# Kernel tuning notes

Measured on AMD Instinct MI355X. Metric: run time of the kernel, lower is better.

## Reference

```python
import jax, jax.numpy as jnp
from jax import lax
import numpy as np

LSTM = 128      # encoder hidden per direction
H2 = 2 * LSTM   # decoder hidden / bi-encoder output dim
E = 1024        # embedding dim
V = 30611       # vocab
A = 64          # attention dim
B, S, T = 16, 400, 96
START_TOK = 101


def setup_inputs() -> dict:
    key = jax.random.key(0)
    ks = jax.random.split(key, 24)
    d = {}
    d["word_embedding"] = jax.random.normal(ks[0], (V, E), jnp.float32) * 0.05
    d["article"] = jax.random.randint(ks[1], (B, S), 0, V)
    d["article_length"] = jax.random.randint(ks[2], (B,), S // 2, S + 1)
    d["abstract"] = jax.random.randint(ks[3], (B, T), 0, V)

    def p(k, shape, scale):
        return jax.random.normal(k, shape, jnp.float32) * scale

    # encoder BiLSTM (PyTorch gate order i,f,g,o), forward and backward dirs
    d["enc_Wih_f"] = p(ks[4], (4 * LSTM, E), 0.03)
    d["enc_Whh_f"] = p(ks[5], (4 * LSTM, LSTM), 0.08)
    d["enc_b_f"] = jnp.zeros((4 * LSTM,), jnp.float32)
    d["enc_Wih_b"] = p(ks[6], (4 * LSTM, E), 0.03)
    d["enc_Whh_b"] = p(ks[7], (4 * LSTM, LSTM), 0.08)
    d["enc_b_b"] = jnp.zeros((4 * LSTM,), jnp.float32)
    # decoder LSTM: input = embed(1024) + context(256)
    d["dec_Wih"] = p(ks[8], (4 * H2, E + H2), 0.03)
    d["dec_Whh"] = p(ks[9], (4 * H2, H2), 0.06)
    d["dec_b"] = jnp.zeros((4 * H2,), jnp.float32)
    # vocab prediction
    d["pred_W"] = p(ks[10], (V, H2), 0.06)
    d["pred_b"] = jnp.zeros((V,), jnp.float32)
    # additive attention
    d["attn_s_W"] = p(ks[11], (A, H2), 0.06)
    d["attn_s_b"] = jnp.zeros((A,), jnp.float32)
    d["attn_h_W"] = p(ks[12], (A, H2), 0.06)
    d["attn_h_b"] = jnp.zeros((A,), jnp.float32)
    d["attn_f_W"] = p(ks[13], (1, A), 0.12)
    d["attn_f_b"] = jnp.zeros((1,), jnp.float32)
    return d


def _lstm_cell(x, h, c, Wih, Whh, b):
    g = x @ Wih.T + h @ Whh.T + b
    i, f, gg, o = jnp.split(g, 4, axis=-1)
    c = jax.nn.sigmoid(f) * c + jax.nn.sigmoid(i) * jnp.tanh(gg)
    h = jax.nn.sigmoid(o) * jnp.tanh(c)
    return h, c


def reference(word_embedding, article, article_length, abstract,
              enc_Wih_f, enc_Whh_f, enc_b_f, enc_Wih_b, enc_Whh_b, enc_b_b,
              dec_Wih, dec_Whh, dec_b, pred_W, pred_b,
              attn_s_W, attn_s_b, attn_h_W, attn_h_b, attn_f_W, attn_f_b):
    dt = word_embedding.dtype
    # ---- encoder ----
    xe = word_embedding[article]          # [B,S,E]
    xs = xe.transpose(1, 0, 2)            # [S,B,E]
    z = jnp.zeros((B, LSTM), dt)

    def fstep(carry, x):
        h, c = carry
        h, c = _lstm_cell(x, h, c, enc_Wih_f, enc_Whh_f, enc_b_f)
        return (h, c), h

    def bstep(carry, x):
        h, c = carry
        h, c = _lstm_cell(x, h, c, enc_Wih_b, enc_Whh_b, enc_b_b)
        return (h, c), h

    (hf, cf_f), out_f = lax.scan(fstep, (z, z), xs)
    (hb, cf_b), out_b = lax.scan(bstep, (z, z), xs, reverse=True)
    enc_out = jnp.concatenate([out_f, out_b], axis=-1).transpose(1, 0, 2)  # [B,S,2H]

    # decoder init state = concat of final fwd/bwd encoder states
    h0 = jnp.concatenate([hf, hb], axis=-1)   # [B,H2]
    c0 = jnp.concatenate([cf_f, cf_b], axis=-1)

    # attention mask: (+9999 valid, -9999 pad); min(score, mask) keeps valid scores
    length = jnp.clip(article_length, 1, S)
    pos = jnp.arange(S)
    mask = jnp.where(pos[None, :] < length[:, None], 9999.0, -9999.0).astype(dt)

    enc_ws = enc_out @ attn_s_W.T + attn_s_b  # [B,S,A], precomputed per original code

    # teacher forcing inputs: step 0 uses token 101, step t uses abstract[:, t-1]
    tokens_in = jnp.concatenate(
        [jnp.full((B, 1), START_TOK, dtype=abstract.dtype), abstract[:, :-1]], axis=1)
    emb_in = word_embedding[tokens_in].transpose(1, 0, 2)  # [T,B,E]

    def dstep(carry, emb):
        h, c, ctx = carry
        x = jnp.concatenate([emb, ctx], axis=-1)           # [B,E+H2]
        h, c = _lstm_cell(x, h, c, dec_Wih, dec_Whh, dec_b)
        logits = h @ pred_W.T + pred_b                     # [B,V]
        wh = h @ attn_h_W.T + attn_h_b                     # [B,A]
        score = jnp.tanh(enc_ws + wh[:, None, :]) @ attn_f_W[0] + attn_f_b[0]  # [B,S]
        score = jnp.minimum(score, mask)
        w = jax.nn.softmax(score, axis=-1)
        ctx = jnp.einsum('bs,bsd->bd', w, enc_out)         # [B,H2]
        return (h, c, ctx), logits

    ctx0 = jnp.zeros((B, H2), dt)
    _, logits = lax.scan(dstep, (h0, c0, ctx0), emb_in)    # [T,B,V]

    logits = logits.transpose(1, 0, 2).reshape(B * T, V)
    tgt = abstract.reshape(-1)
    logp = jax.nn.log_softmax(logits, axis=-1)
    nll = -jnp.take_along_axis(logp, tgt[:, None], axis=1)[:, 0]
    valid = (tgt != 0).astype(logits.dtype)                # ignore_index=0
    loss = jnp.sum(nll * valid) / jnp.maximum(jnp.sum(valid), 1.0)
    return loss
```

## Files before the change

### kernel.cpp

```cpp
#include <hip/hip_runtime.h>
#include <cmath>

#define NB 16
#define SS 400
#define TT 96
#define HL 128
#define HH 256
#define AA 64
#define VV 30611
#define VVP 30720
#define START_TOK 101
#define NCHUNK 120

typedef __attribute__((ext_vector_type(8))) short bf16x8;
typedef __attribute__((ext_vector_type(4))) float f32x4;

#define PIN4(v) asm volatile("" : "+v"((v).x), "+v"((v).y), "+v"((v).z), "+v"((v).w))
#define LBAR() asm volatile("s_waitcnt lgkmcnt(0)\n\ts_barrier" ::: "memory")

__device__ __forceinline__ float gload(const float* p) {
  return __hip_atomic_load(p, __ATOMIC_RELAXED, __HIP_MEMORY_SCOPE_AGENT);
}
__device__ __forceinline__ void gstore(float* p, float v) {
  __hip_atomic_store(p, v, __ATOMIC_RELAXED, __HIP_MEMORY_SCOPE_AGENT);
}
__device__ __forceinline__ float sigmf(float x) { return 1.0f / (1.0f + __expf(-x)); }
__device__ __forceinline__ float tanhf_(float x) {
  float xc = fminf(fmaxf(x, -15.0f), 15.0f);
  return 1.0f - 2.0f / (__expf(2.0f * xc) + 1.0f);
}
__device__ __forceinline__ short f2bf(float f) {
  unsigned u = __float_as_uint(f);
  unsigned r = (u + 0x7FFFu + ((u >> 16) & 1u)) >> 16;
  return (short)r;
}
__device__ __forceinline__ void flagbar(int* flags, int b, int g, int target) {
  __syncthreads();
  if (threadIdx.x == 0)
    __hip_atomic_store(&flags[b*8 + g], target, __ATOMIC_RELAXED, __HIP_MEMORY_SCOPE_AGENT);
  if (threadIdx.x < 8) {
    while (__hip_atomic_load(&flags[b*8 + threadIdx.x], __ATOMIC_RELAXED, __HIP_MEMORY_SCOPE_AGENT) < target)
      __builtin_amdgcn_s_sleep(1);
  }
  LBAR();
}

__global__ __launch_bounds__(256) void k_init(int* flags) {
  if (threadIdx.x < 128) flags[threadIdx.x] = 0;
}

__global__ __launch_bounds__(256) void k_casts(
    const float* __restrict__ predW, const float* __restrict__ wf,
    const float* __restrict__ wb, const float* __restrict__ dwih,
    short* __restrict__ predWb, short* __restrict__ wfB,
    short* __restrict__ wbB, short* __restrict__ dwB)
{
  const int stride = gridDim.x * 256;
  const int t0 = blockIdx.x * 256 + threadIdx.x;
  for (int i = t0; i < VVP*256; i += stride)
    predWb[i] = (i < VV*256) ? f2bf(predW[i]) : (short)0;
  for (int i = t0; i < 512*1024; i += stride) wfB[i] = f2bf(wf[i]);
  for (int i = t0; i < 512*1024; i += stride) wbB[i] = f2bf(wb[i]);
  for (int i = t0; i < 1024*1024; i += stride) {
    int r = i >> 10, k = i & 1023;
    dwB[i] = f2bf(dwih[r*1280 + k]);
  }
}

__global__ __launch_bounds__(256) void k_embproj_enc_mfma(
    const float* __restrict__ emb, const int* __restrict__ article,
    const short* __restrict__ wfB, const short* __restrict__ wbB,
    const float* __restrict__ bf, const float* __restrict__ bb,
    float* __restrict__ xcomb)
{
  const int m0 = blockIdx.x * 64;
  const int n0 = blockIdx.y * 256;
  const int t = threadIdx.x;
  const int w = t >> 6, l = t & 63;
  __shared__ short Abuf[64*136];
  __shared__ int tok[64];
  if (t < 64) {
    int R = m0 + t, s = R >> 4, b = R & 15;
    tok[t] = article[b*SS + s];
  }
  const short* __restrict__ Wb = (n0 < 512) ? wfB : wbB;
  const int nb0 = (n0 < 512) ? n0 : (n0 - 512);
  f32x4 acc[4][4];
  #pragma unroll
  for (int i = 0; i < 4; ++i)
    #pragma unroll
    for (int j = 0; j < 4; ++j) acc[i][j] = (f32x4){0.f,0.f,0.f,0.f};
  __syncthreads();
  const int ar = t >> 2, ak0 = (t & 3) * 32;
  for (int kc = 0; kc < 8; ++kc) {
    const float* src = emb + (size_t)tok[ar]*1024 + kc*128 + ak0;
    #pragma unroll
    for (int j = 0; j < 8; ++j) {
      float4 v = *(const float4*)(src + 4*j);
      short4 s4; s4.x = f2bf(v.x); s4.y = f2bf(v.y); s4.z = f2bf(v.z); s4.w = f2bf(v.w);
      *(short4*)(&Abuf[ar*136 + ak0 + 4*j]) = s4;
    }
    LBAR();
    #pragma unroll
    for (int ks = 0; ks < 4; ++ks) {
      bf16x8 af[4];
      #pragma unroll
      for (int mr = 0; mr < 4; ++mr)
        af[mr] = *(const bf16x8*)(&Abuf[(mr*16 + (l & 15))*136 + ks*32 + (l >> 4)*8]);
      #pragma unroll
      for (int ct = 0; ct < 4; ++ct) {
        int n = nb0 + w*64 + ct*16 + (l & 15);
        bf16x8 bfr = *(const bf16x8*)(Wb + (size_t)n*1024 + kc*128 + ks*32 + (l >> 4)*8);
        #pragma unroll
        for (int mr = 0; mr < 4; ++mr)
          acc[mr][ct] = __builtin_amdgcn_mfma_f32_16x16x32_bf16(af[mr], bfr, acc[mr][ct], 0, 0, 0);
      }
    }
    LBAR();
  }
  #pragma unroll
  for (int ct = 0; ct < 4; ++ct) {
    int n = n0 + w*64 + ct*16 + (l & 15);
    float bias = (n < 512) ? bf[n] : bb[n - 512];
    #pragma unroll
    for (int mr = 0; mr < 4; ++mr) {
      #pragma unroll
      for (int r = 0; r < 4; ++r) {
        int R = m0 + mr*16 + (l >> 4)*4 + r;
        xcomb[(size_t)R*1024 + n] = acc[mr][ct][r] + bias;
      }
    }
  }
}

__global__ __launch_bounds__(256) void k_embproj_dec_mfma(
    const float* __restrict__ emb, const int* __restrict__ abstr,
    const short* __restrict__ dwB, const float* __restrict__ db,
    float* __restrict__ decpre)
{
  const int m0 = blockIdx.x * 64;
  const int n0 = blockIdx.y * 256;
  const int t = threadIdx.x;
  const int w = t >> 6, l = t & 63;
  __shared__ short Abuf[64*136];
  __shared__ int tok[64];
  if (t < 64) {
    int R = m0 + t, tt = R >> 4, b = R & 15;
    tok[t] = (tt == 0) ? START_TOK : abstr[b*TT + tt - 1];
  }
  f32x4 acc[4][4];
  #pragma unroll
  for (int i = 0; i < 4; ++i)
    #pragma unroll
    for (int j = 0; j < 4; ++j) acc[i][j] = (f32x4){0.f,0.f,0.f,0.f};
  __syncthreads();
  const int ar = t >> 2, ak0 = (t & 3) * 32;
  for (int kc = 0; kc < 8; ++kc) {
    const float* src = emb + (size_t)tok[ar]*1024 + kc*128 + ak0;
    #pragma unroll
    for (int j = 0; j < 8; ++j) {
      float4 v = *(const float4*)(src + 4*j);
      short4 s4; s4.x = f2bf(v.x); s4.y = f2bf(v.y); s4.z = f2bf(v.z); s4.w = f2bf(v.w);
      *(short4*)(&Abuf[ar*136 + ak0 + 4*j]) = s4;
    }
    LBAR();
    #pragma unroll
    for (int ks = 0; ks < 4; ++ks) {
      bf16x8 af[4];
      #pragma unroll
      for (int mr = 0; mr < 4; ++mr)
        af[mr] = *(const bf16x8*)(&Abuf[(mr*16 + (l & 15))*136 + ks*32 + (l >> 4)*8]);
      #pragma unroll
      for (int ct = 0; ct < 4; ++ct) {
        int n = n0 + w*64 + ct*16 + (l & 15);
        bf16x8 bfr = *(const bf16x8*)(dwB + (size_t)n*1024 + kc*128 + ks*32 + (l >> 4)*8);
        #pragma unroll
        for (int mr = 0; mr < 4; ++mr)
          acc[mr][ct] = __builtin_amdgcn_mfma_f32_16x16x32_bf16(af[mr], bfr, acc[mr][ct], 0, 0, 0);
      }
    }
    LBAR();
  }
  #pragma unroll
  for (int ct = 0; ct < 4; ++ct) {
    int n = n0 + w*64 + ct*16 + (l & 15);
    float bias = db[n];
    #pragma unroll
    for (int mr = 0; mr < 4; ++mr) {
      #pragma unroll
      for (int r = 0; r < 4; ++r) {
        int R = m0 + mr*16 + (l >> 4)*4 + r;
        decpre[(size_t)R*1024 + n] = acc[mr][ct][r] + bias;
      }
    }
  }
}

__global__ __launch_bounds__(1024, 4) void k_encoder(
    const float* __restrict__ xcomb,
    const float* __restrict__ whhf, const float* __restrict__ whhb,
    float* __restrict__ encout,
    float* __restrict__ hpub,
    float* __restrict__ c0buf)
{
  const int b = blockIdx.x & 15, dir = blockIdx.x >> 4;
  const int t = threadIdx.x;
  const int row = t & 511;
  const int ks = t >> 9;
  const float* __restrict__ Whh = dir ? whhb : whhf;
  float4 wr[16];
  #pragma unroll
  for (int j = 0; j < 16; ++j) {
    wr[j] = *(const float4*)(Whh + row*128 + ks*64 + j*4);
    PIN4(wr[j]);
  }
  __shared__ float hl[128];
  __shared__ float part[2][512];
  float c_reg = 0.0f;
  if (t < 128) hl[t] = 0.0f;
  float xv0 = 0.f, xv1 = 0.f, xv2 = 0.f, xv3 = 0.f;
  if (t < 128) {
    const float* xr = xcomb + ((dir ? (SS-1) : 0)*NB + b)*1024 + dir*512 + t;
    xv0 = xr[0]; xv1 = xr[128]; xv2 = xr[256]; xv3 = xr[384];
  }
  __syncthreads();
  for (int s = 0; s < SS; ++s) {
    const int sf = dir ? (SS-1-s) : s;
    const float* hs = hl + ks*64;
    float a0 = 0.f, a1 = 0.f, a2 = 0.f, a3 = 0.f;
    #pragma unroll
    for (int j = 0; j < 16; j += 4) {
      float4 h0 = *(const float4*)(hs + j*4);
      float4 h1 = *(const float4*)(hs + j*4 + 4);
      float4 h2 = *(const float4*)(hs + j*4 + 8);
      float4 h3 = *(const float4*)(hs + j*4 + 12);
      a0 += wr[j].x*h0.x + wr[j].y*h0.y + wr[j].z*h0.z + wr[j].w*h0.w;
      a1 += wr[j+1].x*h1.x + wr[j+1].y*h1.y + wr[j+1].z*h1.z + wr[j+1].w*h1.w;
      a2 += wr[j+2].x*h2.x + wr[j+2].y*h2.y + wr[j+2].z*h2.z + wr[j+2].w*h2.w;
      a3 += wr[j+3].x*h3.x + wr[j+3].y*h3.y + wr[j+3].z*h3.z + wr[j+3].w*h3.w;
    }
    part[ks][row] = (a0 + a1) + (a2 + a3);
    float nx0 = 0.f, nx1 = 0.f, nx2 = 0.f, nx3 = 0.f;
    if (t < 128 && s + 1 < SS) {
      const int sfn = dir ? (SS-2-s) : (s+1);
      const float* xr = xcomb + (sfn*NB + b)*1024 + dir*512 + t;
      nx0 = xr[0]; nx1 = xr[128]; nx2 = xr[256]; nx3 = xr[384];
    }
    LBAR();
    if (t < 128) {
      float gi = part[0][t]       + part[1][t]       + xv0;
      float gf = part[0][128 + t] + part[1][128 + t] + xv1;
      float gg = part[0][256 + t] + part[1][256 + t] + xv2;
      float go = part[0][384 + t] + part[1][384 + t] + xv3;
      float iv = sigmf(gi), fv = sigmf(gf), gv = tanhf_(gg), ov = sigmf(go);
      c_reg = fv*c_reg + iv*gv;
      float hv = ov*tanhf_(c_reg);
      hl[t] = hv;
      encout[(b*SS + sf)*HH + dir*HL + t] = hv;
    }
    LBAR();
    xv0 = nx0; xv1 = nx1; xv2 = nx2; xv3 = nx3;
  }
  if (t < 128) {
    hpub[b*HH + dir*HL + t] = hl[t];
    c0buf[b*HH + dir*HL + t] = c_reg;
  }
}

__global__ __launch_bounds__(256) void k_encws(
    const float* __restrict__ encout,
    const float* __restrict__ asW, const float* __restrict__ asb,
    float* __restrict__ encwsR)
{
  const int rt = blockIdx.x;
  const int tid = threadIdx.x;
  __shared__ float Al[32*260];
  #pragma unroll
  for (int i = 0; i < 32; ++i) {
    int l = tid + i*256;
    int r = l >> 8, k = l & 255;
    Al[r*260 + k] = encout[(rt*32 + r)*256 + k];
  }
  __syncthreads();
  const int a = tid & 63, rg = tid >> 6;
  float acc[8];
  #pragma unroll
  for (int q = 0; q < 8; ++q) acc[q] = 0.0f;
  const float4* w4 = (const float4*)(asW + a*256);
  for (int k4 = 0; k4 < 64; ++k4) {
    float4 w = w4[k4];
    #pragma unroll
    for (int q = 0; q < 8; ++q) {
      const float4* a4 = (const float4*)(Al + (rg*8 + q)*260);
      float4 av = a4[k4];
      acc[q] += av.x*w.x + av.y*w.y + av.z*w.z + av.w*w.w;
    }
  }
  float bias = asb[a];
  #pragma unroll
  for (int q = 0; q < 8; ++q) {
    int row = rt*32 + rg*8 + q;
    encwsR[row*64 + a] = acc[q] + bias;
  }
}

__global__ __launch_bounds__(1024, 4) void k_decoder(
    const float* __restrict__ decpre,
    const float* __restrict__ dwhh,
    const float* __restrict__ dwih,
    const float* __restrict__ ahW, const float* __restrict__ ahb,
    const float* __restrict__ afW, const float* __restrict__ afb,
    const float* __restrict__ encwsR,
    const float* __restrict__ encout,
    const int* __restrict__ alen,
    const float* __restrict__ c0buf,
    float* hpub,
    float* cpub,
    float* wpub,
    float* __restrict__ dhall,
    int* flags)
{
  const int wg = blockIdx.x;
  const int g = wg >> 4, b = wg & 15;
  const int t = threadIdx.x;
  const int r = t & 127, ks = t >> 7;
  const int lane = t & 63;
  const int u = t & 31;
  const int s0 = g*50;

  const int grow = (r >> 5)*256 + g*32 + (r & 31);
  float4 wr[16];
  #pragma unroll
  for (int j = 0; j < 16; ++j) {
    int k = ks*64 + j*4;
    wr[j] = (k < 256) ? *(const float4*)(dwhh + grow*256 + k)
                      : *(const float4*)(dwih + grow*1280 + 1024 + (k - 256));
    PIN4(wr[j]);
  }

  __shared__ float encl[50*256];
  __shared__ float wsl[50*68];
  __shared__ float ahWt[256*68];
  __shared__ float hc[512];
  __shared__ float part[8][132];
  __shared__ float wh[64];
  __shared__ float fwl[64];
  __shared__ float scl[64];
  __shared__ float sh_m, sh_s;

  for (int i = t; i < 50*256; i += 1024) {
    int si = i >> 8, d = i & 255;
    encl[i] = encout[(b*SS + s0 + si)*HH + d];
  }
  for (int i = t; i < 50*64; i += 1024) {
    int si = i >> 6, a = i & 63;
    wsl[si*68 + a] = encwsR[(b*SS + s0 + si)*64 + a];
  }
  for (int i = t; i < 64*256; i += 1024) {
    int a = i >> 8, k = i & 255;
    ahWt[k*68 + a] = ahW[i];
  }
  if (t < 64) fwl[t] = afW[t];
  const float fb0 = afb[0];
  int len = alen[b]; len = min(max(len, 1), SS);
  float c_reg = 0.f;
  float pre0 = 0.f, pre1 = 0.f, pre2 = 0.f, pre3 = 0.f;
  if (t < 256) {
    c_reg = c0buf[b*HH + g*32 + u];
    hc[t] = gload(hpub + b*HH + t);
    hc[256 + t] = 0.0f;
    const float* pr = decpre + (size_t)(0*NB + b)*1024 + g*32 + u;
    pre0 = pr[0]; pre1 = pr[256]; pre2 = pr[512]; pre3 = pr[768];
  }
  __syncthreads();

  for (int tt = 0; tt < TT; ++tt) {
    {
      const float* hs = hc + ks*64;
      float a0 = 0.f, a1 = 0.f, a2 = 0.f, a3 = 0.f;
      #pragma unroll
      for (int j = 0; j < 16; j += 4) {
        float4 h0 = *(const float4*)(hs + j*4);
        float4 h1 = *(const float4*)(hs + j*4 + 4);
        float4 h2 = *(const float4*)(hs + j*4 + 8);
        float4 h3 = *(const float4*)(hs + j*4 + 12);
        a0 += wr[j].x*h0.x + wr[j].y*h0.y + wr[j].z*h0.z + wr[j].w*h0.w;
        a1 += wr[j+1].x*h1.x + wr[j+1].y*h1.y + wr[j+1].z*h1.z + wr[j+1].w*h1.w;
        a2 += wr[j+2].x*h2.x + wr[j+2].y*h2.y + wr[j+2].z*h2.z + wr[j+2].w*h2.w;
        a3 += wr[j+3].x*h3.x + wr[j+3].y*h3.y + wr[j+3].z*h3.z + wr[j+3].w*h3.w;
      }
      part[ks][r] = (a0 + a1) + (a2 + a3);
    }
    LBAR();
    if (t < 256) {
      float g0 = pre0, g1 = pre1, g2 = pre2, g3 = pre3;
      #pragma unroll
      for (int j = 0; j < 8; ++j) {
        g0 += part[j][u];
        g1 += part[j][32 + u];
        g2 += part[j][64 + u];
        g3 += part[j][96 + u];
      }
      float iv = sigmf(g0), fv = sigmf(g1), gv = tanhf_(g2), ov = sigmf(g3);
      c_reg = fv*c_reg + iv*gv;
      float hv = ov*tanhf_(c_reg);
      if (t < 32) {
        gstore(hpub + b*HH + g*32 + t, hv);
        dhall[(tt*NB + b)*HH + g*32 + t] = hv;
      }
      int wv = t >> 6;
      int a = wv*16 + (lane >> 2);
      int j4 = lane & 3;
      float wacc = 0.f;
      #pragma unroll
      for (int i = 0; i < 8; ++i) {
        int u2 = j4*8 + i;
        float hx = __shfl(hv, u2, 64);
        wacc += ahWt[(g*32 + u2)*68 + a] * hx;
      }
      wacc += __shfl_xor(wacc, 1);
      wacc += __shfl_xor(wacc, 2);
      if (j4 == 0) gstore(wpub + (b*8 + g)*72 + a, wacc);
    }
    flagbar(flags, b, g, 2*tt + 1);
    if (t < 256) {
      hc[t] = gload(hpub + b*HH + t);
      if (tt + 1 < TT) {
        const float* pr = decpre + (size_t)((tt+1)*NB + b)*1024 + g*32 + u;
        pre0 = pr[0]; pre1 = pr[256]; pre2 = pr[512]; pre3 = pr[768];
      }
    } else if (t < 320) {
      int a = t - 256;
      float s = ahb[a];
      #pragma unroll
      for (int j = 0; j < 8; ++j) s += gload(wpub + (b*8 + j)*72 + a);
      wh[a] = s;
    }
    LBAR();
    if (t < 800) {
      int s = t >> 4, j = t & 15;
      const float* wrow = wsl + s*68 + j*4;
      float p = fwl[j*4]   * tanhf_(wrow[0] + wh[j*4])
              + fwl[j*4+1] * tanhf_(wrow[1] + wh[j*4+1])
              + fwl[j*4+2] * tanhf_(wrow[2] + wh[j*4+2])
              + fwl[j*4+3] * tanhf_(wrow[3] + wh[j*4+3]);
      p += __shfl_xor(p, 1);
      p += __shfl_xor(p, 2);
      p += __shfl_xor(p, 4);
      p += __shfl_xor(p, 8);
      if (j == 0) scl[s] = p;
    }
    LBAR();
    if (t < 64) {
      float sc = -1e30f;
      if (t < 50) {
        sc = fb0 + scl[t];
        sc = fminf(sc, (s0 + t < len) ? 9999.0f : -9999.0f);
      }
      float m = sc;
      #pragma unroll
      for (int o = 32; o; o >>= 1) m = fmaxf(m, __shfl_xor(m, o));
      float p = (t < 50) ? __expf(sc - m) : 0.0f;
      scl[t] = p;
      float ssum = p;
      #pragma unroll
      for (int o = 32; o; o >>= 1) ssum += __shfl_xor(ssum, o);
      if (t == 0) { sh_m = m; sh_s = ssum; }
    }
    LBAR();
    if (t < 256) {
      float acc = 0.0f;
      const float* eb = encl + t;
      #pragma unroll 10
      for (int i = 0; i < 50; ++i) acc += scl[i] * eb[i*256];
      gstore(cpub + (b*8 + g)*272 + t, acc);
      if (t == 0) gstore(cpub + (b*8 + g)*272 + 256, sh_m);
      if (t == 1) gstore(cpub + (b*8 + g)*272 + 257, sh_s);
    }
    flagbar(flags, b, g, 2*tt + 2);
    if (t < 256) {
      float mj[8], sj[8];
      #pragma unroll
      for (int j = 0; j < 8; ++j) {
        mj[j] = gload(cpub + (b*8 + j)*272 + 256);
        sj[j] = gload(cpub + (b*8 + j)*272 + 257);
      }
      float M = mj[0];
      #pragma unroll
      for (int j = 1; j < 8; ++j) M = fmaxf(M, mj[j]);
      float denom = 0.f, ctx = 0.f;
      #pragma unroll
      for (int j = 0; j < 8; ++j) {
        float e = __expf(mj[j] - M);
        denom += sj[j] * e;
        ctx += gload(cpub + (b*8 + j)*272 + t) * e;
      }
      hc[256 + t] = ctx / denom;
    }
    LBAR();
  }
}

__global__ __launch_bounds__(256) void k_pred_mfma(
    const float* __restrict__ dhall,
    const short* __restrict__ predWb,
    const float* __restrict__ predb,
    float* __restrict__ pm, float* __restrict__ ps)
{
  const int m0 = blockIdx.x * 64;
  const int ch = blockIdx.y;
  const int c0 = ch * 256;
  const int t = threadIdx.x;
  const int w = t >> 6, l = t & 63;
  __shared__ __align__(16) char smem[64*264*4];
  short* Abuf = (short*)smem;
  float* L    = (float*)smem;
  __shared__ float red[256];
  __shared__ float rowmax[64];

  {
    const int ar = t >> 2, ak0 = (t & 3) * 64;
    const float* src = dhall + (size_t)(m0 + ar)*256 + ak0;
    #pragma unroll
    for (int j = 0; j < 16; ++j) {
      float4 v = *(const float4*)(src + 4*j);
      short4 s4; s4.x = f2bf(v.x); s4.y = f2bf(v.y); s4.z = f2bf(v.z); s4.w = f2bf(v.w);
      *(short4*)(&Abuf[ar*264 + ak0 + 4*j]) = s4;
    }
  }
  LBAR();
  f32x4 acc[4][4];
  #pragma unroll
  for (int i = 0; i < 4; ++i)
    #pragma unroll
    for (int j = 0; j < 4; ++j) acc[i][j] = (f32x4){0.f,0.f,0.f,0.f};
  #pragma unroll
  for (int kst = 0; kst < 8; ++kst) {
    bf16x8 af[4];
    #pragma unroll
    for (int mr = 0; mr < 4; ++mr)
      af[mr] = *(const bf16x8*)(&Abuf[(mr*16 + (l & 15))*264 + kst*32 + (l >> 4)*8]);
    #pragma unroll
    for (int ct = 0; ct < 4; ++ct) {
      int col = c0 + w*64 + ct*16 + (l & 15);
      bf16x8 bfr = *(const bf16x8*)(predWb + (size_t)col*256 + kst*32 + (l >> 4)*8);
      #pragma unroll
      for (int mr = 0; mr < 4; ++mr)
        acc[mr][ct] = __builtin_amdgcn_mfma_f32_16x16x32_bf16(af[mr], bfr, acc[mr][ct], 0, 0, 0);
    }
  }
  LBAR();
  #pragma unroll
  for (int ct = 0; ct < 4; ++ct) {
    int col = c0 + w*64 + ct*16 + (l & 15);
    float bias = (col < VV) ? predb[col] : 0.0f;
    bool valid = (col < VV);
    #pragma unroll
    for (int mr = 0; mr < 4; ++mr) {
      #pragma unroll
      for (int r = 0; r < 4; ++r) {
        int rl = mr*16 + (l >> 4)*4 + r;
        L[rl*264 + w*64 + ct*16 + (l & 15)] = valid ? (acc[mr][ct][r] + bias) : -1e30f;
      }
    }
  }
  LBAR();
  {
    const int row = t & 63, qd = t >> 6;
    float m = -1e30f;
    const float* Lr = L + row*264 + qd*64;
    for (int i = 0; i < 64; ++i) m = fmaxf(m, Lr[i]);
    red[qd*64 + row] = m;
  }
  LBAR();
  if (t < 64) {
    float m = fmaxf(fmaxf(red[t], red[64+t]), fmaxf(red[128+t], red[192+t]));
    rowmax[t] = m;
  }
  LBAR();
  {
    const int row = t & 63, qd = t >> 6;
    float m = rowmax[row];
    float ssum = 0.f;
    const float* Lr = L + row*264 + qd*64;
    for (int i = 0; i < 64; ++i) ssum += __expf(Lr[i] - m);
    red[qd*64 + row] = ssum;
  }
  LBAR();
  if (t < 64) {
    float ssum = red[t] + red[64+t] + red[128+t] + red[192+t];
    pm[(m0 + t)*NCHUNK + ch] = rowmax[t];
    ps[(m0 + t)*NCHUNK + ch] = ssum;
  }
}

__global__ __launch_bounds__(256) void k_loss_part(
    const float* __restrict__ pm, const float* __restrict__ ps,
    const float* __restrict__ dhall,
    const float* __restrict__ predW, const float* __restrict__ predb,
    const int* __restrict__ abstr, float* __restrict__ lpart)
{
  const int tid = threadIdx.x;
  const int row = blockIdx.x*256 + tid;
  __shared__ float rs[256], rc[256];
  float lsum = 0.0f, lcnt = 0.0f;
  {
    int t = row >> 4, b = row & 15;
    int tok = abstr[b*TT + t];
    float m = -1e30f;
    for (int c = 0; c < NCHUNK; ++c) m = fmaxf(m, pm[row*NCHUNK + c]);
    float ss = 0.0f;
    for (int c = 0; c < NCHUNK; ++c) ss += ps[row*NCHUNK + c] * __expf(pm[row*NCHUNK + c] - m);
    float lse = m + __logf(ss);
    float tl = predb[tok];
    const float* hrow = dhall + row*256;
    const float* wrow = predW + tok*256;
    #pragma unroll 4
    for (int k = 0; k < 256; ++k) tl += hrow[k] * wrow[k];
    if (tok != 0) { lsum = lse - tl; lcnt = 1.0f; }
  }
  rs[tid] = lsum; rc[tid] = lcnt;
  __syncthreads();
  for (int st = 128; st; st >>= 1) {
    if (tid < st) { rs[tid] += rs[tid + st]; rc[tid] += rc[tid + st]; }
    __syncthreads();
  }
  if (tid == 0) { lpart[blockIdx.x*2] = rs[0]; lpart[blockIdx.x*2 + 1] = rc[0]; }
}

__global__ void k_loss_final(const float* __restrict__ lpart, float* __restrict__ out) {
  if (threadIdx.x == 0) {
    float s = 0.f, c = 0.f;
    for (int i = 0; i < 6; ++i) { s += lpart[i*2]; c += lpart[i*2 + 1]; }
    out[0] = s / fmaxf(c, 1.0f);
  }
}

extern "C" void kernel_launch(void* const* d_in, const int* in_sizes, int n_in,
                              void* d_out, int out_size, void* d_ws, size_t ws_size,
                              hipStream_t stream) {
  const float* emb   = (const float*)d_in[0];
  const int* article = (const int*)d_in[1];
  const int* alen    = (const int*)d_in[2];
  const int* abstr   = (const int*)d_in[3];
  const float* eWihF = (const float*)d_in[4];
  const float* eWhhF = (const float*)d_in[5];
  const float* ebF   = (const float*)d_in[6];
  const float* eWihB = (const float*)d_in[7];
  const float* eWhhB = (const float*)d_in[8];
  const float* ebB   = (const float*)d_in[9];
  const float* dWih  = (const float*)d_in[10];
  const float* dWhh  = (const float*)d_in[11];
  const float* db    = (const float*)d_in[12];
  const float* pW    = (const float*)d_in[13];
  const float* pb    = (const float*)d_in[14];
  const float* asW   = (const float*)d_in[15];
  const float* asb   = (const float*)d_in[16];
  const float* ahW   = (const float*)d_in[17];
  const float* ahb   = (const float*)d_in[18];
  const float* afW   = (const float*)d_in[19];
  const float* afb   = (const float*)d_in[20];
  float* out = (float*)d_out;

  float* w = (float*)d_ws;
  size_t o = 0;
  float* xcomb  = w + o; o += (size_t)SS*NB*1024;
  float* encout = w + o; o += (size_t)NB*SS*HH;
  float* encwsR = w + o; o += (size_t)NB*SS*AA;
  float* decpre = w + o; o += (size_t)TT*NB*1024;
  float* dhall  = w + o; o += (size_t)TT*NB*HH;
  float* hpub   = w + o; o += NB*HH;
  float* cpub   = w + o; o += NB*8*272;
  float* wpub   = w + o; o += NB*8*72;
  float* c0buf  = w + o; o += NB*HH;
  float* pm     = w + o; o += (size_t)TT*NB*NCHUNK;
  float* ps     = w + o; o += (size_t)TT*NB*NCHUNK;
  float* lpart  = w + o; o += 16;
  int* flags = (int*)(w + o); o += 128;
  short* predWb = (short*)(w + o); o += (size_t)VVP*256/2;
  short* wfB    = (short*)(w + o); o += 512*1024/2;
  short* wbB    = (short*)(w + o); o += 512*1024/2;
  short* dwB    = (short*)(w + o); o += 1024*1024/2;

  k_init<<<1, 256, 0, stream>>>(flags);
  k_casts<<<2048, 256, 0, stream>>>(pW, eWihF, eWihB, dWih, predWb, wfB, wbB, dwB);
  k_embproj_enc_mfma<<<dim3(100, 4), 256, 0, stream>>>(emb, article, wfB, wbB, ebF, ebB, xcomb);
  k_embproj_dec_mfma<<<dim3(24, 4), 256, 0, stream>>>(emb, abstr, dwB, db, decpre);
  k_encoder<<<32, 1024, 0, stream>>>(xcomb, eWhhF, eWhhB, encout, hpub, c0buf);
  k_encws<<<200, 256, 0, stream>>>(encout, asW, asb, encwsR);
  k_decoder<<<128, 1024, 0, stream>>>(decpre, dWhh, dWih, ahW, ahb, afW, afb,
                                      encwsR, encout, alen, c0buf, hpub, cpub, wpub, dhall, flags);
  k_pred_mfma<<<dim3(24, 120), 256, 0, stream>>>(dhall, predWb, pb, pm, ps);
  k_loss_part<<<6, 256, 0, stream>>>(pm, ps, dhall, pW, pb, abstr, lpart);
  k_loss_final<<<1, 64, 0, stream>>>(lpart, out);
}
```

Measured before the change: 1.715 ms.

## Overlap vocab projection with decoder via flag-synced persistent blocks; shuffle-based encoder cell

```diff
diff --git a/kernel.cpp b/kernel.cpp
--- a/kernel.cpp
+++ b/kernel.cpp
@@ -19,6 +19,9 @@
 #define LBAR() asm volatile("s_waitcnt lgkmcnt(0)\n\ts_barrier" ::: "memory")
 
 __device__ __forceinline__ float gload(const float* p) {
+  return __hip_atomic_load(p, __ATOMIC_RELAXED, __HIP_MEMORY_SCOPE_AGENT);
+}
+__device__ __forceinline__ int gload_i(const int* p) {
   return __hip_atomic_load(p, __ATOMIC_RELAXED, __HIP_MEMORY_SCOPE_AGENT);
 }
 __device__ __forceinline__ void gstore(float* p, float v) {
@@ -205,28 +208,28 @@
 {
   const int b = blockIdx.x & 15, dir = blockIdx.x >> 4;
   const int t = threadIdx.x;
-  const int row = t & 511;
-  const int ks = t >> 9;
+  const int w = t >> 6, lane = t & 63;
+  const int kh = lane >> 5;
+  const int gate = (lane >> 3) & 3;
+  const int ul = lane & 7;
+  const int u = w*8 + ul;
+  const int row = gate*128 + u;
   const float* __restrict__ Whh = dir ? whhb : whhf;
   float4 wr[16];
   #pragma unroll
   for (int j = 0; j < 16; ++j) {
-    wr[j] = *(const float4*)(Whh + row*128 + ks*64 + j*4);
+    wr[j] = *(const float4*)(Whh + row*128 + kh*64 + j*4);
     PIN4(wr[j]);
   }
-  __shared__ float hl[128];
-  __shared__ float part[2][512];
-  float c_reg = 0.0f;
-  if (t < 128) hl[t] = 0.0f;
-  float xv0 = 0.f, xv1 = 0.f, xv2 = 0.f, xv3 = 0.f;
-  if (t < 128) {
-    const float* xr = xcomb + ((dir ? (SS-1) : 0)*NB + b)*1024 + dir*512 + t;
-    xv0 = xr[0]; xv1 = xr[128]; xv2 = xr[256]; xv3 = xr[384];
-  }
+  __shared__ float hl[2][128];
+  if (t < 128) hl[0][t] = 0.0f;
+  float c_reg = 0.0f, hlast = 0.0f;
+  float xv = xcomb[((dir ? (SS-1) : 0)*NB + b)*1024 + dir*512 + row];
   __syncthreads();
+  int p = 0;
   for (int s = 0; s < SS; ++s) {
     const int sf = dir ? (SS-1-s) : s;
-    const float* hs = hl + ks*64;
+    const float* hs = hl[p] + kh*64;
     float a0 = 0.f, a1 = 0.f, a2 = 0.f, a3 = 0.f;
     #pragma unroll
     for (int j = 0; j < 16; j += 4) {
@@ -239,31 +242,31 @@
       a2 += wr[j+2].x*h2.x + wr[j+2].y*h2.y + wr[j+2].z*h2.z + wr[j+2].w*h2.w;
       a3 += wr[j+3].x*h3.x + wr[j+3].y*h3.y + wr[j+3].z*h3.z + wr[j+3].w*h3.w;
     }
-    part[ks][row] = (a0 + a1) + (a2 + a3);
-    float nx0 = 0.f, nx1 = 0.f, nx2 = 0.f, nx3 = 0.f;
-    if (t < 128 && s + 1 < SS) {
+    float acc = (a0 + a1) + (a2 + a3);
+    float nxv = 0.f;
+    if (s + 1 < SS) {
       const int sfn = dir ? (SS-2-s) : (s+1);
-      const float* xr = xcomb + (sfn*NB + b)*1024 + dir*512 + t;
-      nx0 = xr[0]; nx1 = xr[128]; nx2 = xr[256]; nx3 = xr[384];
-    }
-    LBAR();
-    if (t < 128) {
-      float gi = part[0][t]       + part[1][t]       + xv0;
-      float gf = part[0][128 + t] + part[1][128 + t] + xv1;
-      float gg = part[0][256 + t] + part[1][256 + t] + xv2;
-      float go = part[0][384 + t] + part[1][384 + t] + xv3;
-      float iv = sigmf(gi), fv = sigmf(gf), gv = tanhf_(gg), ov = sigmf(go);
+      nxv = xcomb[(sfn*NB + b)*1024 + dir*512 + row];
+    }
+    float full = acc + __shfl_xor(acc, 32) + xv;
+    float gf = __shfl(full, 8 + ul);
+    float gg = __shfl(full, 16 + ul);
+    float go = __shfl(full, 24 + ul);
+    if (lane < 8) {
+      float iv = sigmf(full), fv = sigmf(gf), gv = tanhf_(gg), ov = sigmf(go);
       c_reg = fv*c_reg + iv*gv;
       float hv = ov*tanhf_(c_reg);
-      hl[t] = hv;
-      encout[(b*SS + sf)*HH + dir*HL + t] = hv;
+      hl[p^1][u] = hv;
+      hlast = hv;
+      encout[(b*SS + sf)*HH + dir*HL + u] = hv;
     }
     LBAR();
-    xv0 = nx0; xv1 = nx1; xv2 = nx2; xv3 = nx3;
-  }
-  if (t < 128) {
-    hpub[b*HH + dir*HL + t] = hl[t];
-    c0buf[b*HH + dir*HL + t] = c_reg;
+    p ^= 1;
+    xv = nxv;
+  }
+  if (lane < 8) {
+    hpub[b*HH + dir*HL + u] = hlast;
+    c0buf[b*HH + dir*HL + u] = c_reg;
   }
 }
 
@@ -304,7 +307,7 @@
   }
 }
 
-__global__ __launch_bounds__(1024, 4) void k_decoder(
+__global__ __launch_bounds__(1024, 4) void k_decoder_pred(
     const float* __restrict__ decpre,
     const float* __restrict__ dwhh,
     const float* __restrict__ dwih,
@@ -314,283 +317,282 @@
     const float* __restrict__ encout,
     const int* __restrict__ alen,
     const float* __restrict__ c0buf,
-    float* hpub,
-    float* cpub,
-    float* wpub,
+    float* hpub, float* cpub, float* wpub,
     float* __restrict__ dhall,
-    int* flags)
-{
-  const int wg = blockIdx.x;
-  const int g = wg >> 4, b = wg & 15;
-  const int t = threadIdx.x;
-  const int r = t & 127, ks = t >> 7;
-  const int lane = t & 63;
-  const int u = t & 31;
-  const int s0 = g*50;
-
-  const int grow = (r >> 5)*256 + g*32 + (r & 31);
-  float4 wr[16];
-  #pragma unroll
-  for (int j = 0; j < 16; ++j) {
-    int k = ks*64 + j*4;
-    wr[j] = (k < 256) ? *(const float4*)(dwhh + grow*256 + k)
-                      : *(const float4*)(dwih + grow*1280 + 1024 + (k - 256));
-    PIN4(wr[j]);
-  }
-
-  __shared__ float encl[50*256];
-  __shared__ float wsl[50*68];
-  __shared__ float ahWt[256*68];
-  __shared__ float hc[512];
-  __shared__ float part[8][132];
-  __shared__ float wh[64];
-  __shared__ float fwl[64];
-  __shared__ float scl[64];
-  __shared__ float sh_m, sh_s;
-
-  for (int i = t; i < 50*256; i += 1024) {
-    int si = i >> 8, d = i & 255;
-    encl[i] = encout[(b*SS + s0 + si)*HH + d];
-  }
-  for (int i = t; i < 50*64; i += 1024) {
-    int si = i >> 6, a = i & 63;
-    wsl[si*68 + a] = encwsR[(b*SS + s0 + si)*64 + a];
-  }
-  for (int i = t; i < 64*256; i += 1024) {
-    int a = i >> 8, k = i & 255;
-    ahWt[k*68 + a] = ahW[i];
-  }
-  if (t < 64) fwl[t] = afW[t];
-  const float fb0 = afb[0];
-  int len = alen[b]; len = min(max(len, 1), SS);
-  float c_reg = 0.f;
-  float pre0 = 0.f, pre1 = 0.f, pre2 = 0.f, pre3 = 0.f;
-  if (t < 256) {
-    c_reg = c0buf[b*HH + g*32 + u];
-    hc[t] = gload(hpub + b*HH + t);
-    hc[256 + t] = 0.0f;
-    const float* pr = decpre + (size_t)(0*NB + b)*1024 + g*32 + u;
-    pre0 = pr[0]; pre1 = pr[256]; pre2 = pr[512]; pre3 = pr[768];
-  }
-  __syncthreads();
-
-  for (int tt = 0; tt < TT; ++tt) {
-    {
-      const float* hs = hc + ks*64;
-      float a0 = 0.f, a1 = 0.f, a2 = 0.f, a3 = 0.f;
-      #pragma unroll
-      for (int j = 0; j < 16; j += 4) {
-        float4 h0 = *(const float4*)(hs + j*4);
-        float4 h1 = *(const float4*)(hs + j*4 + 4);
-        float4 h2 = *(const float4*)(hs + j*4 + 8);
-        float4 h3 = *(const float4*)(hs + j*4 + 12);
-        a0 += wr[j].x*h0.x + wr[j].y*h0.y + wr[j].z*h0.z + wr[j].w*h0.w;
-        a1 += wr[j+1].x*h1.x + wr[j+1].y*h1.y + wr[j+1].z*h1.z + wr[j+1].w*h1.w;
-        a2 += wr[j+2].x*h2.x + wr[j+2].y*h2.y + wr[j+2].z*h2.z + wr[j+2].w*h2.w;
-        a3 += wr[j+3].x*h3.x + wr[j+3].y*h3.y + wr[j+3].z*h3.z + wr[j+3].w*h3.w;
-      }
-      part[ks][r] = (a0 + a1) + (a2 + a3);
-    }
-    LBAR();
-    if (t < 256) {
-      float g0 = pre0, g1 = pre1, g2 = pre2, g3 = pre3;
-      #pragma unroll
-      for (int j = 0; j < 8; ++j) {
-        g0 += part[j][u];
-        g1 += part[j][32 + u];
-        g2 += part[j][64 + u];
-        g3 += part[j][96 + u];
-      }
-      float iv = sigmf(g0), fv = sigmf(g1), gv = tanhf_(g2), ov = sigmf(g3);
-      c_reg = fv*c_reg + iv*gv;
-      float hv = ov*tanhf_(c_reg);
-      if (t < 32) {
-        gstore(hpub + b*HH + g*32 + t, hv);
-        dhall[(tt*NB + b)*HH + g*32 + t] = hv;
-      }
-      int wv = t >> 6;
-      int a = wv*16 + (lane >> 2);
-      int j4 = lane & 3;
-      float wacc = 0.f;
-      #pragma unroll
-      for (int i = 0; i < 8; ++i) {
-        int u2 = j4*8 + i;
-        float hx = __shfl(hv, u2, 64);
-        wacc += ahWt[(g*32 + u2)*68 + a] * hx;
-      }
-      wacc += __shfl_xor(wacc, 1);
-      wacc += __shfl_xor(wacc, 2);
-      if (j4 == 0) gstore(wpub + (b*8 + g)*72 + a, wacc);
-    }
-    flagbar(flags, b, g, 2*tt + 1);
-    if (t < 256) {
-      hc[t] = gload(hpub + b*HH + t);
-      if (tt + 1 < TT) {
-        const float* pr = decpre + (size_t)((tt+1)*NB + b)*1024 + g*32 + u;
-        pre0 = pr[0]; pre1 = pr[256]; pre2 = pr[512]; pre3 = pr[768];
-      }
-    } else if (t < 320) {
-      int a = t - 256;
-      float s = ahb[a];
-      #pragma unroll
-      for (int j = 0; j < 8; ++j) s += gload(wpub + (b*8 + j)*72 + a);
-      wh[a] = s;
-    }
-    LBAR();
-    if (t < 800) {
-      int s = t >> 4, j = t & 15;
-      const float* wrow = wsl + s*68 + j*4;
-      float p = fwl[j*4]   * tanhf_(wrow[0] + wh[j*4])
-              + fwl[j*4+1] * tanhf_(wrow[1] + wh[j*4+1])
-              + fwl[j*4+2] * tanhf_(wrow[2] + wh[j*4+2])
-              + fwl[j*4+3] * tanhf_(wrow[3] + wh[j*4+3]);
-      p += __shfl_xor(p, 1);
-      p += __shfl_xor(p, 2);
-      p += __shfl_xor(p, 4);
-      p += __shfl_xor(p, 8);
-      if (j == 0) scl[s] = p;
-    }
-    LBAR();
-    if (t < 64) {
-      float sc = -1e30f;
-      if (t < 50) {
-        sc = fb0 + scl[t];
-        sc = fminf(sc, (s0 + t < len) ? 9999.0f : -9999.0f);
-      }
-      float m = sc;
-      #pragma unroll
-      for (int o = 32; o; o >>= 1) m = fmaxf(m, __shfl_xor(m, o));
-      float p = (t < 50) ? __expf(sc - m) : 0.0f;
-      scl[t] = p;
-      float ssum = p;
-      #pragma unroll
-      for (int o = 32; o; o >>= 1) ssum += __shfl_xor(ssum, o);
-      if (t == 0) { sh_m = m; sh_s = ssum; }
-    }
-    LBAR();
-    if (t < 256) {
-      float acc = 0.0f;
-      const float* eb = encl + t;
-      #pragma unroll 10
-      for (int i = 0; i < 50; ++i) acc += scl[i] * eb[i*256];
-      gstore(cpub + (b*8 + g)*272 + t, acc);
-      if (t == 0) gstore(cpub + (b*8 + g)*272 + 256, sh_m);
-      if (t == 1) gstore(cpub + (b*8 + g)*272 + 257, sh_s);
-    }
-    flagbar(flags, b, g, 2*tt + 2);
-    if (t < 256) {
-      float mj[8], sj[8];
-      #pragma unroll
-      for (int j = 0; j < 8; ++j) {
-        mj[j] = gload(cpub + (b*8 + j)*272 + 256);
-        sj[j] = gload(cpub + (b*8 + j)*272 + 257);
-      }
-      float M = mj[0];
-      #pragma unroll
-      for (int j = 1; j < 8; ++j) M = fmaxf(M, mj[j]);
-      float denom = 0.f, ctx = 0.f;
-      #pragma unroll
-      for (int j = 0; j < 8; ++j) {
-        float e = __expf(mj[j] - M);
-        denom += sj[j] * e;
-        ctx += gload(cpub + (b*8 + j)*272 + t) * e;
-      }
-      hc[256 + t] = ctx / denom;
-    }
-    LBAR();
-  }
-}
-
-__global__ __launch_bounds__(256) void k_pred_mfma(
-    const float* __restrict__ dhall,
+    int* flags,
     const short* __restrict__ predWb,
     const float* __restrict__ predb,
     float* __restrict__ pm, float* __restrict__ ps)
 {
-  const int m0 = blockIdx.x * 64;
-  const int ch = blockIdx.y;
-  const int c0 = ch * 256;
+  __shared__ __align__(16) float smem[35372];
   const int t = threadIdx.x;
-  const int w = t >> 6, l = t & 63;
-  __shared__ __align__(16) char smem[64*264*4];
-  short* Abuf = (short*)smem;
-  float* L    = (float*)smem;
-  __shared__ float red[256];
-  __shared__ float rowmax[64];
-
-  {
-    const int ar = t >> 2, ak0 = (t & 3) * 64;
-    const float* src = dhall + (size_t)(m0 + ar)*256 + ak0;
+
+  if (blockIdx.x < 128) {
+    float* encl = smem;
+    float* wsl  = smem + 12800;
+    float* ahWt = smem + 16200;
+    float* hc   = smem + 33608;
+    float* part = smem + 34120;
+    float* wh   = smem + 35176;
+    float* fwl  = smem + 35240;
+    float* scl  = smem + 35304;
+    float* shms = smem + 35368;
+
+    const int wg = blockIdx.x;
+    const int g = wg >> 4, b = wg & 15;
+    const int r = t & 127, ks = t >> 7;
+    const int lane = t & 63;
+    const int u = t & 31;
+    const int s0 = g*50;
+    const int grow = (r >> 5)*256 + g*32 + (r & 31);
+    float4 wr[16];
     #pragma unroll
     for (int j = 0; j < 16; ++j) {
-      float4 v = *(const float4*)(src + 4*j);
-      short4 s4; s4.x = f2bf(v.x); s4.y = f2bf(v.y); s4.z = f2bf(v.z); s4.w = f2bf(v.w);
-      *(short4*)(&Abuf[ar*264 + ak0 + 4*j]) = s4;
-    }
-  }
-  LBAR();
-  f32x4 acc[4][4];
-  #pragma unroll
-  for (int i = 0; i < 4; ++i)
-    #pragma unroll
-    for (int j = 0; j < 4; ++j) acc[i][j] = (f32x4){0.f,0.f,0.f,0.f};
-  #pragma unroll
-  for (int kst = 0; kst < 8; ++kst) {
-    bf16x8 af[4];
-    #pragma unroll
-    for (int mr = 0; mr < 4; ++mr)
-      af[mr] = *(const bf16x8*)(&Abuf[(mr*16 + (l & 15))*264 + kst*32 + (l >> 4)*8]);
-    #pragma unroll
-    for (int ct = 0; ct < 4; ++ct) {
-      int col = c0 + w*64 + ct*16 + (l & 15);
-      bf16x8 bfr = *(const bf16x8*)(predWb + (size_t)col*256 + kst*32 + (l >> 4)*8);
-      #pragma unroll
-      for (int mr = 0; mr < 4; ++mr)
-        acc[mr][ct] = __builtin_amdgcn_mfma_f32_16x16x32_bf16(af[mr], bfr, acc[mr][ct], 0, 0, 0);
-    }
-  }
-  LBAR();
-  #pragma unroll
-  for (int ct = 0; ct < 4; ++ct) {
-    int col = c0 + w*64 + ct*16 + (l & 15);
-    float bias = (col < VV) ? predb[col] : 0.0f;
-    bool valid = (col < VV);
-    #pragma unroll
-    for (int mr = 0; mr < 4; ++mr) {
-      #pragma unroll
-      for (int r = 0; r < 4; ++r) {
-        int rl = mr*16 + (l >> 4)*4 + r;
-        L[rl*264 + w*64 + ct*16 + (l & 15)] = valid ? (acc[mr][ct][r] + bias) : -1e30f;
-      }
-    }
-  }
-  LBAR();
-  {
-    const int row = t & 63, qd = t >> 6;
-    float m = -1e30f;
-    const float* Lr = L + row*264 + qd*64;
-    for (int i = 0; i < 64; ++i) m = fmaxf(m, Lr[i]);
-    red[qd*64 + row] = m;
-  }
-  LBAR();
-  if (t < 64) {
-    float m = fmaxf(fmaxf(red[t], red[64+t]), fmaxf(red[128+t], red[192+t]));
-    rowmax[t] = m;
-  }
-  LBAR();
-  {
-    const int row = t & 63, qd = t >> 6;
-    float m = rowmax[row];
-    float ssum = 0.f;
-    const float* Lr = L + row*264 + qd*64;
-    for (int i = 0; i < 64; ++i) ssum += __expf(Lr[i] - m);
-    red[qd*64 + row] = ssum;
-  }
-  LBAR();
-  if (t < 64) {
-    float ssum = red[t] + red[64+t] + red[128+t] + red[192+t];
-    pm[(m0 + t)*NCHUNK + ch] = rowmax[t];
-    ps[(m0 + t)*NCHUNK + ch] = ssum;
+      int k = ks*64 + j*4;
+      wr[j] = (k < 256) ? *(const float4*)(dwhh + grow*256 + k)
+                        : *(const float4*)(dwih + grow*1280 + 1024 + (k - 256));
+      PIN4(wr[j]);
+    }
+    for (int i = t; i < 50*256; i += 1024) {
+      int si = i >> 8, d = i & 255;
+      encl[i] = encout[(b*SS + s0 + si)*HH + d];
+    }
+    for (int i = t; i < 50*64; i += 1024) {
+      int si = i >> 6, a = i & 63;
+      wsl[si*68 + a] = encwsR[(b*SS + s0 + si)*64 + a];
+    }
+    for (int i = t; i < 64*256; i += 1024) {
+      int a = i >> 8, k = i & 255;
+      ahWt[k*68 + a] = ahW[i];
+    }
+    if (t < 64) fwl[t] = afW[t];
+    const float fb0 = afb[0];
+    int len = alen[b]; len = min(max(len, 1), SS);
+    float c_reg = 0.f;
+    float pre0 = 0.f, pre1 = 0.f, pre2 = 0.f, pre3 = 0.f;
+    if (t < 256) {
+      c_reg = c0buf[b*HH + g*32 + u];
+      hc[t] = gload(hpub + b*HH + t);
+      hc[256 + t] = 0.0f;
+      const float* pr = decpre + (size_t)(0*NB + b)*1024 + g*32 + u;
+      pre0 = pr[0]; pre1 = pr[256]; pre2 = pr[512]; pre3 = pr[768];
+    }
+    __syncthreads();
+
+    for (int tt = 0; tt < TT; ++tt) {
+      {
+        const float* hs = hc + ks*64;
+        float a0 = 0.f, a1 = 0.f, a2 = 0.f, a3 = 0.f;
+        #pragma unroll
+        for (int j = 0; j < 16; j += 4) {
+          float4 h0 = *(const float4*)(hs + j*4);
+          float4 h1 = *(const float4*)(hs + j*4 + 4);
+          float4 h2 = *(const float4*)(hs + j*4 + 8);
+          float4 h3 = *(const float4*)(hs + j*4 + 12);
+          a0 += wr[j].x*h0.x + wr[j].y*h0.y + wr[j].z*h0.z + wr[j].w*h0.w;
+          a1 += wr[j+1].x*h1.x + wr[j+1].y*h1.y + wr[j+1].z*h1.z + wr[j+1].w*h1.w;
+          a2 += wr[j+2].x*h2.x + wr[j+2].y*h2.y + wr[j+2].z*h2.z + wr[j+2].w*h2.w;
+          a3 += wr[j+3].x*h3.x + wr[j+3].y*h3.y + wr[j+3].z*h3.z + wr[j+3].w*h3.w;
+        }
+        part[ks*132 + r] = (a0 + a1) + (a2 + a3);
+      }
+      LBAR();
+      if (t < 256) {
+        float g0 = pre0, g1 = pre1, g2 = pre2, g3 = pre3;
+        #pragma unroll
+        for (int j = 0; j < 8; ++j) {
+          g0 += part[j*132 + u];
+          g1 += part[j*132 + 32 + u];
+          g2 += part[j*132 + 64 + u];
+          g3 += part[j*132 + 96 + u];
+        }
+        float iv = sigmf(g0), fv = sigmf(g1), gv = tanhf_(g2), ov = sigmf(g3);
+        c_reg = fv*c_reg + iv*gv;
+        float hv = ov*tanhf_(c_reg);
+        if (t < 32) {
+          gstore(hpub + b*HH + g*32 + t, hv);
+          gstore(dhall + (size_t)(tt*NB + b)*HH + g*32 + t, hv);
+        }
+        int wv = t >> 6;
+        int a = wv*16 + (lane >> 2);
+        int j4 = lane & 3;
+        float wacc = 0.f;
+        #pragma unroll
+        for (int i = 0; i < 8; ++i) {
+          int u2 = j4*8 + i;
+          float hx = __shfl(hv, u2, 64);
+          wacc += ahWt[(g*32 + u2)*68 + a] * hx;
+        }
+        wacc += __shfl_xor(wacc, 1);
+        wacc += __shfl_xor(wacc, 2);
+        if (j4 == 0) gstore(wpub + (b*8 + g)*72 + a, wacc);
+      }
+      flagbar(flags, b, g, 2*tt + 1);
+      if (t < 256) {
+        hc[t] = gload(hpub + b*HH + t);
+        if (tt + 1 < TT) {
+          const float* pr = decpre + (size_t)((tt+1)*NB + b)*1024 + g*32 + u;
+          pre0 = pr[0]; pre1 = pr[256]; pre2 = pr[512]; pre3 = pr[768];
+        }
+      } else if (t < 320) {
+        int a = t - 256;
+        float s = ahb[a];
+        #pragma unroll
+        for (int j = 0; j < 8; ++j) s += gload(wpub + (b*8 + j)*72 + a);
+        wh[a] = s;
+      }
+      LBAR();
+      if (t < 800) {
+        int s = t >> 4, j = t & 15;
+        const float* wrow = wsl + s*68 + j*4;
+        float p = fwl[j*4]   * tanhf_(wrow[0] + wh[j*4])
+                + fwl[j*4+1] * tanhf_(wrow[1] + wh[j*4+1])
+                + fwl[j*4+2] * tanhf_(wrow[2] + wh[j*4+2])
+                + fwl[j*4+3] * tanhf_(wrow[3] + wh[j*4+3]);
+        p += __shfl_xor(p, 1);
+        p += __shfl_xor(p, 2);
+        p += __shfl_xor(p, 4);
+        p += __shfl_xor(p, 8);
+        if (j == 0) scl[s] = p;
+      }
+      LBAR();
+      if (t < 64) {
+        float sc = -1e30f;
+        if (t < 50) {
+          sc = fb0 + scl[t];
+          sc = fminf(sc, (s0 + t < len) ? 9999.0f : -9999.0f);
+        }
+        float m = sc;
+        #pragma unroll
+        for (int o = 32; o; o >>= 1) m = fmaxf(m, __shfl_xor(m, o));
+        float p = (t < 50) ? __expf(sc - m) : 0.0f;
+        scl[t] = p;
+        float ssum = p;
+        #pragma unroll
+        for (int o = 32; o; o >>= 1) ssum += __shfl_xor(ssum, o);
+        if (t == 0) { shms[0] = m; shms[1] = ssum; }
+      }
+      LBAR();
+      if (t < 256) {
+        float acc = 0.0f;
+        const float* eb = encl + t;
+        #pragma unroll 10
+        for (int i = 0; i < 50; ++i) acc += scl[i] * eb[i*256];
+        gstore(cpub + (b*8 + g)*272 + t, acc);
+        if (t == 0) gstore(cpub + (b*8 + g)*272 + 256, shms[0]);
+        if (t == 1) gstore(cpub + (b*8 + g)*272 + 257, shms[1]);
+      }
+      flagbar(flags, b, g, 2*tt + 2);
+      if (t < 256) {
+        float mj[8], sj[8];
+        #pragma unroll
+        for (int j = 0; j < 8; ++j) {
+          mj[j] = gload(cpub + (b*8 + j)*272 + 256);
+          sj[j] = gload(cpub + (b*8 + j)*272 + 257);
+        }
+        float M = mj[0];
+        #pragma unroll
+        for (int j = 1; j < 8; ++j) M = fmaxf(M, mj[j]);
+        float denom = 0.f, ctx = 0.f;
+        #pragma unroll
+        for (int j = 0; j < 8; ++j) {
+          float e = __expf(mj[j] - M);
+          denom += sj[j] * e;
+          ctx += gload(cpub + (b*8 + j)*272 + t) * e;
+        }
+        hc[256 + t] = ctx / denom;
+      }
+      LBAR();
+    }
+  } else {
+    short* Abuf = (short*)smem;
+    float* L    = smem;
+    float* red  = smem + 16896;
+    float* rowmax = smem + 17920;
+    const int hw = blockIdx.x - 128;
+    const int w = t >> 6, l = t & 63;
+
+    for (int k = 0; k < 23; ++k) {
+      int item = hw + 128*k;
+      if (item >= 24*120) break;
+      int tt4 = item / 120, ch = item - tt4*120;
+      int m0 = tt4*64, c0 = ch*256;
+      int target = 2*(tt4*4 + 3) + 1;
+      if (t < 128)
+        while (gload_i(flags + t) < target) __builtin_amdgcn_s_sleep(16);
+      __syncthreads();
+      #pragma unroll
+      for (int j = 0; j < 16; ++j) {
+        int e = t + j*1024;
+        int row = e >> 8, col = e & 255;
+        Abuf[row*264 + col] = f2bf(gload(dhall + (size_t)(m0 + row)*256 + col));
+      }
+      LBAR();
+      f32x4 acc[4];
+      #pragma unroll
+      for (int i = 0; i < 4; ++i) acc[i] = (f32x4){0.f,0.f,0.f,0.f};
+      #pragma unroll
+      for (int kst = 0; kst < 8; ++kst) {
+        bf16x8 af[4];
+        #pragma unroll
+        for (int mr = 0; mr < 4; ++mr)
+          af[mr] = *(const bf16x8*)(&Abuf[(mr*16 + (l & 15))*264 + kst*32 + (l >> 4)*8]);
+        int col = c0 + w*16 + (l & 15);
+        bf16x8 bfr = *(const bf16x8*)(predWb + (size_t)col*256 + kst*32 + (l >> 4)*8);
+        #pragma unroll
+        for (int mr = 0; mr < 4; ++mr)
+          acc[mr] = __builtin_amdgcn_mfma_f32_16x16x32_bf16(af[mr], bfr, acc[mr], 0, 0, 0);
+      }
+      LBAR();
+      {
+        int col = c0 + w*16 + (l & 15);
+        float bias = (col < VV) ? predb[col] : 0.0f;
+        bool valid = (col < VV);
+        #pragma unroll
+        for (int mr = 0; mr < 4; ++mr) {
+          #pragma unroll
+          for (int rr = 0; rr < 4; ++rr) {
+            int rl = mr*16 + (l >> 4)*4 + rr;
+            L[rl*264 + w*16 + (l & 15)] = valid ? (acc[mr][rr] + bias) : -1e30f;
+          }
+        }
+      }
+      LBAR();
+      {
+        const int row = t & 63, qd = t >> 6;
+        float m = -1e30f;
+        const float* Lr = L + row*264 + qd*16;
+        #pragma unroll
+        for (int i = 0; i < 16; ++i) m = fmaxf(m, Lr[i]);
+        red[qd*64 + row] = m;
+      }
+      LBAR();
+      if (t < 64) {
+        float m = -1e30f;
+        #pragma unroll
+        for (int qd = 0; qd < 16; ++qd) m = fmaxf(m, red[qd*64 + t]);
+        rowmax[t] = m;
+      }
+      LBAR();
+      {
+        const int row = t & 63, qd = t >> 6;
+        float m = rowmax[row];
+        float ssum = 0.f;
+        const float* Lr = L + row*264 + qd*16;
+        #pragma unroll
+        for (int i = 0; i < 16; ++i) ssum += __expf(Lr[i] - m);
+        red[qd*64 + row] = ssum;
+      }
+      LBAR();
+      if (t < 64) {
+        float ssum = 0.f;
+        #pragma unroll
+        for (int qd = 0; qd < 16; ++qd) ssum += red[qd*64 + t];
+        pm[(m0 + t)*NCHUNK + ch] = rowmax[t];
+        ps[(m0 + t)*NCHUNK + ch] = ssum;
+      }
+      LBAR();
+    }
   }
 }
 
@@ -688,9 +690,9 @@
   k_embproj_dec_mfma<<<dim3(24, 4), 256, 0, stream>>>(emb, abstr, dwB, db, decpre);
   k_encoder<<<32, 1024, 0, stream>>>(xcomb, eWhhF, eWhhB, encout, hpub, c0buf);
   k_encws<<<200, 256, 0, stream>>>(encout, asW, asb, encwsR);
-  k_decoder<<<128, 1024, 0, stream>>>(decpre, dWhh, dWih, ahW, ahb, afW, afb,
-                                      encwsR, encout, alen, c0buf, hpub, cpub, wpub, dhall, flags);
-  k_pred_mfma<<<dim3(24, 120), 256, 0, stream>>>(dhall, predWb, pb, pm, ps);
+  k_decoder_pred<<<256, 1024, 0, stream>>>(decpre, dWhh, dWih, ahW, ahb, afW, afb,
+                                           encwsR, encout, alen, c0buf, hpub, cpub, wpub,
+                                           dhall, flags, predWb, pb, pm, ps);
   k_loss_part<<<6, 256, 0, stream>>>(pm, ps, dhall, pW, pb, abstr, lpart);
   k_loss_final<<<1, 64, 0, stream>>>(lpart, out);
 }
```

Result: slower. 2.075 ms (+21.0%).
